# Performance work log

Hardware: AMD Instinct MI355X
Metric: run time of the kernel (lower is better)

The kernel has to match this reference:

```python
import jax, jax.numpy as jnp
import numpy as np

B = 128  # batch of (adv, clean) image pairs; each image is (3, 32, 32)


def setup_inputs() -> dict:
    key = jax.random.key(0)
    k1, k2 = jax.random.split(key)
    return {
        "adver_image": jax.random.normal(k1, (B, 3, 32, 32), dtype=jnp.float32),
        "clean_image": jax.random.normal(k2, (B, 3, 32, 32), dtype=jnp.float32),
    }


def _img2patch(img):
    # (3,32,32) -> (64,3,4,4): 8x8 grid of 4x4 patches (matches view+permute in torch)
    return img.reshape(3, 8, 4, 8, 4).transpose(1, 3, 0, 2, 4).reshape(64, 3, 4, 4)


def _patches2imgs(p):
    # (64,64,3,4,4) -> (64,3,32,32): inverse of _img2patch, batched over the 64 attacks
    return p.reshape(64, 8, 8, 3, 4, 4).transpose(0, 3, 1, 4, 2, 5).reshape(64, 3, 32, 32)


def _recon(amp, pha):
    # amplitude * exp(i*phase), ifft over the 4x4 patch dims, magnitude
    return jnp.abs(jnp.fft.ifft2(amp * jnp.exp(1j * pha), axes=(-2, -1)))


def _attack_one(adv, cle):
    adv_p = _img2patch(adv)  # (64,3,4,4)
    cle_p = _img2patch(cle)
    f_adv = jnp.fft.fft2(adv_p, axes=(-2, -1))
    f_cle = jnp.fft.fft2(cle_p, axes=(-2, -1))
    A_amp, A_pha = jnp.abs(f_adv), jnp.angle(f_adv)
    C_amp, C_pha = jnp.abs(f_cle), jnp.angle(f_cle)

    # Faithful to torch `_replace`: replace values EQUAL to the idx-th patch's values.
    # Vectorized over all 64 idx at once -> (64,64,3,4,4)
    swap_pha = jax.vmap(lambda loc: jnp.where(C_pha == loc[None], A_pha, C_pha))(C_pha)
    phase_attack = _patches2imgs(_recon(C_amp[None], swap_pha))  # (64,3,32,32)

    swap_amp = jax.vmap(lambda loc: jnp.where(C_amp == loc[None], A_amp, C_amp))(C_amp)
    amplitude_attack = _patches2imgs(_recon(swap_amp, C_pha[None]))  # (64,3,32,32)
    return phase_attack, amplitude_attack


def reference(adver_image, clean_image):
    # -> (PhaseAttack (B,64,3,32,32), AmplitudeAttack (B,64,3,32,32))
    return jax.vmap(_attack_one)(adver_image, clean_image)
```

## Files before the change

### kernel.cpp

```cpp
#include <hip/hip_runtime.h>
#include <math.h>

static constexpr int HALF_OUT = 128 * 64 * 3 * 32 * 32;

typedef float floatx4 __attribute__((ext_vector_type(4)));

__device__ __forceinline__ float fsqrt(float x) { return __builtin_amdgcn_sqrtf(x); }
__device__ __forceinline__ float frcp(float x)  { return __builtin_amdgcn_rcpf(x); }

__device__ __forceinline__ void ifft_real_store(const float zre[16], const float zim[16],
                                                float* __restrict__ obase) {
    float gr[4][4], gi1[4], gi3[4];
    #pragma unroll
    for (int rr = 0; rr < 2; ++rr) {
        const int ku = rr * 2, b0 = ku * 4;
        float t0r = zre[b0+0] + zre[b0+2];
        float t1r = zre[b0+0] - zre[b0+2];
        float t2r = zre[b0+1] + zre[b0+3];
        float t3i = zim[b0+1] - zim[b0+3];
        gr[ku][0] = t0r + t2r; gr[ku][2] = t0r - t2r;
        gr[ku][1] = t1r - t3i; gr[ku][3] = t1r + t3i;
    }
    #pragma unroll
    for (int rr = 0; rr < 2; ++rr) {
        const int ku = rr * 2 + 1, b0 = ku * 4;
        float* gi = (rr == 0) ? gi1 : gi3;
        float t0r = zre[b0+0] + zre[b0+2], t0i = zim[b0+0] + zim[b0+2];
        float t1r = zre[b0+0] - zre[b0+2], t1i = zim[b0+0] - zim[b0+2];
        float t2r = zre[b0+1] + zre[b0+3], t2i = zim[b0+1] + zim[b0+3];
        float t3r = zre[b0+1] - zre[b0+3], t3i = zim[b0+1] - zim[b0+3];
        gr[ku][0] = t0r + t2r; gi[0] = t0i + t2i;
        gr[ku][2] = t0r - t2r; gi[2] = t0i - t2i;
        gr[ku][1] = t1r - t3i; gi[1] = t1i + t3r;
        gr[ku][3] = t1r + t3i; gi[3] = t1i - t3r;
    }
    float ov[4][4];
    #pragma unroll
    for (int v = 0; v < 4; ++v) {
        float a  = gr[0][v] + gr[2][v];
        float bq = gr[0][v] - gr[2][v];
        float cq = gr[1][v] + gr[3][v];
        float e  = gi3[v] - gi1[v];
        ov[0][v] = fabsf(a + cq);
        ov[2][v] = fabsf(a - cq);
        ov[1][v] = fabsf(bq + e);
        ov[3][v] = fabsf(bq - e);
    }
    #pragma unroll
    for (int u = 0; u < 4; ++u) {
        floatx4 w4 = { ov[u][0], ov[u][1], ov[u][2], ov[u][3] };
        *reinterpret_cast<floatx4*>(obase + u * 32) = w4;
    }
}

__global__ __launch_bounds__(256, 3) void freqpsr_kernel(
    const float* __restrict__ adv,
    const float* __restrict__ cle,
    float* __restrict__ out)
{
    __shared__ float2 sA   [16][64];
    __shared__ float2 sC   [16][64];
    __shared__ float  sCamp[16][64];
    __shared__ float  sCpha[16][64];
    __shared__ float2 sZA  [16][64];
    __shared__ float  sRatB[16][64];

    const int blk  = blockIdx.x;
    const int type = blk & 1;
    const int bc   = blk >> 1;
    const int b    = bc / 3;
    const int c    = bc % 3;
    const int tid  = threadIdx.x;

    if (tid < 128) {
        const int p   = tid & 63;
        const int img = tid >> 6;
        const float* src = (img ? adv : cle) + ((size_t)b * 3 + c) * 1024;
        const int py = p >> 3, px = p & 7;

        float x[4][4];
        #pragma unroll
        for (int u = 0; u < 4; ++u) {
            float4 r4 = *reinterpret_cast<const float4*>(src + (py * 4 + u) * 32 + px * 4);
            x[u][0] = r4.x; x[u][1] = r4.y; x[u][2] = r4.z; x[u][3] = r4.w;
        }
        float wr[4][4], wi[4][4];
        #pragma unroll
        for (int u = 0; u < 4; ++u) {
            float t0 = x[u][0] + x[u][2], t1 = x[u][0] - x[u][2];
            float t2 = x[u][1] + x[u][3], t3 = x[u][1] - x[u][3];
            wr[u][0] = t0 + t2; wi[u][0] = 0.0f;
            wr[u][2] = t0 - t2; wi[u][2] = 0.0f;
            wr[u][1] = t1;      wi[u][1] = -t3;
            wr[u][3] = t1;      wi[u][3] =  t3;
        }
        float zr[4][4], zi[4][4];
        #pragma unroll
        for (int kv = 0; kv < 4; ++kv) {
            float t0r = wr[0][kv] + wr[2][kv], t0i = wi[0][kv] + wi[2][kv];
            float t1r = wr[0][kv] - wr[2][kv], t1i = wi[0][kv] - wi[2][kv];
            float t2r = wr[1][kv] + wr[3][kv], t2i = wi[1][kv] + wi[3][kv];
            float t3r = wr[1][kv] - wr[3][kv], t3i = wi[1][kv] - wi[3][kv];
            zr[0][kv] = t0r + t2r; zi[0][kv] = t0i + t2i;
            zr[2][kv] = t0r - t2r; zi[2][kv] = t0i - t2i;
            zr[1][kv] = t1r + t3i; zi[1][kv] = t1i - t3r;
            zr[3][kv] = t1r - t3i; zi[3][kv] = t1i + t3r;
        }
        if (img == 0) {
            #pragma unroll
            for (int k = 0; k < 16; ++k) {
                float re = zr[k >> 2][k & 3], im = zi[k >> 2][k & 3];
                sC[k][p]    = make_float2(re * 0.0625f, im * 0.0625f);
                sCamp[k][p] = fsqrt(re * re + im * im);
                sCpha[k][p] = atan2f(im, re);
            }
        } else {
            #pragma unroll
            for (int k = 0; k < 16; ++k)
                sA[k][p] = make_float2(zr[k >> 2][k & 3], zi[k >> 2][k & 3]);
        }
    }
    __syncthreads();

    for (int item = tid; item < 1024; item += 256) {
        const int k = item >> 6, p = item & 63;
        float2 a = sA[k][p];
        float aamp = fsqrt(a.x * a.x + a.y * a.y);
        float camp = sCamp[k][p];
        float2 za;
        if (aamp > 0.0f) { float s = camp * 0.0625f * frcp(aamp); za = make_float2(s * a.x, s * a.y); }
        else             { za = make_float2(camp * 0.0625f, 0.0f); }
        sZA[k][p]   = za;
        sRatB[k][p] = (camp > 0.0f) ? (aamp * frcp(camp)) : 0.0f;
    }
    __syncthreads();

    const int wave = tid >> 6;
    const int p    = tid & 63;
    const int py   = p >> 3, px = p & 7;

    float ccr[16], cci[16];
    #pragma unroll
    for (int k = 0; k < 16; ++k) { float2 cc = sC[k][p]; ccr[k] = cc.x; cci[k] = cc.y; }

    float* const obase0 = out + (size_t)(type ? HALF_OUT : 0)
                              + ((((size_t)b * 64) * 3 + c) << 10)
                              + py * 128 + px * 4;

    if (type == 0) {
        float cphar[16], zar[16], zai[16];
        #pragma unroll
        for (int k = 0; k < 16; ++k) {
            cphar[k] = sCpha[k][p];
            float2 za = sZA[k][p]; zar[k] = za.x; zai[k] = za.y;
        }
        for (int j = 0; j < 16; ++j) {
            const int i = wave * 16 + j;
            float zre[16], zim[16];
            #pragma unroll
            for (int k = 0; k < 16; ++k) {
                float att = sCpha[k][i];
                bool sw = (cphar[k] == att);
                zre[k] = sw ? zar[k] : ccr[k];
                if (k != 0 && k != 2 && k != 8 && k != 10)
                    zim[k] = sw ? zai[k] : cci[k];
            }
            zim[0] = zim[2] = zim[8] = zim[10] = 0.0f;
            ifft_real_store(zre, zim, obase0 + (size_t)i * 3072);
        }
    } else {
        float campr[16], ratr[16];
        #pragma unroll
        for (int k = 0; k < 16; ++k) { campr[k] = sCamp[k][p]; ratr[k] = sRatB[k][p]; }
        for (int j = 0; j < 16; ++j) {
            const int i = wave * 16 + j;
            float zre[16], zim[16];
            #pragma unroll
            for (int k = 0; k < 16; ++k) {
                float att = sCamp[k][i];
                float r = (campr[k] == att) ? ratr[k] : 1.0f;
                zre[k] = r * ccr[k];
                if (k != 0 && k != 2 && k != 8 && k != 10)
                    zim[k] = r * cci[k];
            }
            zim[0] = zim[2] = zim[8] = zim[10] = 0.0f;
            ifft_real_store(zre, zim, obase0 + (size_t)i * 3072);
        }
    }
}

extern "C" void kernel_launch(void* const* d_in, const int* in_sizes, int n_in,
                              void* d_out, int out_size, void* d_ws, size_t ws_size,
                              hipStream_t stream) {
    const float* adv = (const float*)d_in[0];
    const float* cle = (const float*)d_in[1];
    float* out = (float*)d_out;
    (void)in_sizes; (void)n_in; (void)out_size; (void)d_ws; (void)ws_size;

    dim3 grid(128 * 3 * 2);
    dim3 block(256);
    freqpsr_kernel<<<grid, block, 0, stream>>>(adv, cle, out);
}
```

Before: 38.21 us.

## Spread amplitude/phase computation across all threads and add transposed LDS tables

Clean-image amplitude and phase are no longer computed by only 64 threads. All 256 threads now compute them in the second phase, with each thread handling 4 bins of one patch. Real-valued bins (DC and Nyquist) get their phase by a sign test instead of atan2f. Transposed copies of the clean phase and amplitude are stored so the main loop can read the 16 attack values for patch i as four 128-bit broadcast LDS loads instead of 16 scalar loads. The cost is extra shared memory, which may reduce occupancy, and a sign-test phase that must match atan2 bit-exactly (including ±0 cases).

```diff
diff --git a/kernel.cpp b/kernel.cpp
--- a/kernel.cpp
+++ b/kernel.cpp
@@ -7,6 +7,8 @@
 
 __device__ __forceinline__ float fsqrt(float x) { return __builtin_amdgcn_sqrtf(x); }
 __device__ __forceinline__ float frcp(float x)  { return __builtin_amdgcn_rcpf(x); }
+
+#define PI_F 3.14159274101257324f
 
 __device__ __forceinline__ void ifft_real_store(const float zre[16], const float zim[16],
                                                 float* __restrict__ obase) {
@@ -58,12 +60,14 @@
     const float* __restrict__ cle,
     float* __restrict__ out)
 {
-    __shared__ float2 sA   [16][64];
-    __shared__ float2 sC   [16][64];
-    __shared__ float  sCamp[16][64];
-    __shared__ float  sCpha[16][64];
-    __shared__ float2 sZA  [16][64];
-    __shared__ float  sRatB[16][64];
+    __shared__ float2 sA    [16][64];
+    __shared__ float2 sC    [16][64];
+    __shared__ float  sCamp [16][64];
+    __shared__ float  sCpha [16][64];
+    __shared__ float2 sZA   [16][64];
+    __shared__ float  sRatB [16][64];
+    __shared__ float  sCphaT[64][16];
+    __shared__ float  sCampT[64][16];
 
     const int blk  = blockIdx.x;
     const int type = blk & 1;
@@ -108,12 +112,8 @@
         }
         if (img == 0) {
             #pragma unroll
-            for (int k = 0; k < 16; ++k) {
-                float re = zr[k >> 2][k & 3], im = zi[k >> 2][k & 3];
-                sC[k][p]    = make_float2(re * 0.0625f, im * 0.0625f);
-                sCamp[k][p] = fsqrt(re * re + im * im);
-                sCpha[k][p] = atan2f(im, re);
-            }
+            for (int k = 0; k < 16; ++k)
+                sC[k][p] = make_float2(zr[k >> 2][k & 3], zi[k >> 2][k & 3]);
         } else {
             #pragma unroll
             for (int k = 0; k < 16; ++k)
@@ -122,16 +122,31 @@
     }
     __syncthreads();
 
-    for (int item = tid; item < 1024; item += 256) {
-        const int k = item >> 6, p = item & 63;
-        float2 a = sA[k][p];
-        float aamp = fsqrt(a.x * a.x + a.y * a.y);
-        float camp = sCamp[k][p];
-        float2 za;
-        if (aamp > 0.0f) { float s = camp * 0.0625f * frcp(aamp); za = make_float2(s * a.x, s * a.y); }
-        else             { za = make_float2(camp * 0.0625f, 0.0f); }
-        sZA[k][p]   = za;
-        sRatB[k][p] = (camp > 0.0f) ? (aamp * frcp(camp)) : 0.0f;
+    {
+        const int p2 = tid >> 2;
+        const int k4 = (tid & 3) * 4;
+        float phaq[4], ampq[4];
+        #pragma unroll
+        for (int n = 0; n < 4; ++n) {
+            const int k = k4 + n;
+            float2 cc = sC[k][p2];
+            float2 a  = sA[k][p2];
+            float camp = fsqrt(cc.x * cc.x + cc.y * cc.y);
+            bool realbin = (k == 0) | (k == 2) | (k == 8) | (k == 10);
+            float cpha = realbin ? (cc.x < 0.0f ? PI_F : 0.0f) : atan2f(cc.y, cc.x);
+            float aamp = fsqrt(a.x * a.x + a.y * a.y);
+            float2 za;
+            if (aamp > 0.0f) { float s = camp * 0.0625f * frcp(aamp); za = make_float2(s * a.x, s * a.y); }
+            else             { za = make_float2(camp * 0.0625f, 0.0f); }
+            sCamp[k][p2] = camp;
+            sCpha[k][p2] = cpha;
+            sZA[k][p2]   = za;
+            sRatB[k][p2] = (camp > 0.0f) ? (aamp * frcp(camp)) : 0.0f;
+            sC[k][p2]    = make_float2(cc.x * 0.0625f, cc.y * 0.0625f);
+            phaq[n] = cpha; ampq[n] = camp;
+        }
+        *reinterpret_cast<floatx4*>(&sCphaT[p2][k4]) = floatx4{ phaq[0], phaq[1], phaq[2], phaq[3] };
+        *reinterpret_cast<floatx4*>(&sCampT[p2][k4]) = floatx4{ ampq[0], ampq[1], ampq[2], ampq[3] };
     }
     __syncthreads();
 
@@ -156,11 +171,15 @@
         }
         for (int j = 0; j < 16; ++j) {
             const int i = wave * 16 + j;
+            const floatx4* prow = reinterpret_cast<const floatx4*>(&sCphaT[i][0]);
+            floatx4 a0 = prow[0], a1 = prow[1], a2 = prow[2], a3 = prow[3];
+            float att[16];
+            #pragma unroll
+            for (int n = 0; n < 4; ++n) { att[n] = a0[n]; att[4+n] = a1[n]; att[8+n] = a2[n]; att[12+n] = a3[n]; }
             float zre[16], zim[16];
             #pragma unroll
             for (int k = 0; k < 16; ++k) {
-                float att = sCpha[k][i];
-                bool sw = (cphar[k] == att);
+                bool sw = (cphar[k] == att[k]);
                 zre[k] = sw ? zar[k] : ccr[k];
                 if (k != 0 && k != 2 && k != 8 && k != 10)
                     zim[k] = sw ? zai[k] : cci[k];
@@ -174,11 +193,15 @@
         for (int k = 0; k < 16; ++k) { campr[k] = sCamp[k][p]; ratr[k] = sRatB[k][p]; }
         for (int j = 0; j < 16; ++j) {
             const int i = wave * 16 + j;
+            const floatx4* prow = reinterpret_cast<const floatx4*>(&sCampT[i][0]);
+            floatx4 a0 = prow[0], a1 = prow[1], a2 = prow[2], a3 = prow[3];
+            float att[16];
+            #pragma unroll
+            for (int n = 0; n < 4; ++n) { att[n] = a0[n]; att[4+n] = a1[n]; att[8+n] = a2[n]; att[12+n] = a3[n]; }
             float zre[16], zim[16];
             #pragma unroll
             for (int k = 0; k < 16; ++k) {
-                float att = sCamp[k][i];
-                float r = (campr[k] == att) ? ratr[k] : 1.0f;
+                float r = (campr[k] == att[k]) ? ratr[k] : 1.0f;
                 zre[k] = r * ccr[k];
                 if (k != 0 && k != 2 && k != 8 && k != 10)
                     zim[k] = r * cci[k];
```

New measurement: 37.70 us, median of 2. About the same (-1.3%).
